# Optimization experiments

Hardware: AMD Instinct MI355X
Metric: run time of the kernel (lower is better)

## Reference

```python
import jax, jax.numpy as jnp
import numpy as np

B, N, C = 4, 20480, 128
H, HD = 8, 16           # num_heads, head_dim (C // H)
L = 4                   # number of WindowBasedGraphAttentionBlocks
NW, WS = 320, 64        # num_windows, window_size (N // NW)
SCALE = HD ** -0.5
EPS = 1e-5


def layernorm(x, g, b):
    mu = jnp.mean(x, axis=-1, keepdims=True)
    var = jnp.mean(jnp.square(x - mu), axis=-1, keepdims=True)
    return (x - mu) * jax.lax.rsqrt(var + EPS) * g + b


def setup_inputs() -> dict:
    key = jax.random.key(0)
    ks = jax.random.split(key, 8)
    x = jax.random.normal(ks[0], (B, N, C), dtype=jnp.float32)
    # geodesic window mapping: each of NW windows has exactly WS members, permuted
    window_ids = jnp.asarray(
        np.random.RandomState(0).permutation(np.repeat(np.arange(NW), WS)),
        dtype=jnp.int32)
    s = 0.02
    inp = {
        'x': x,
        'g1': jnp.ones((L, C), jnp.float32),
        'be1': jnp.zeros((L, C), jnp.float32),
        'Wqkv': jax.random.normal(ks[1], (L, C, 3 * C), jnp.float32) * s,
        'bqkv': jnp.zeros((L, 3 * C), jnp.float32),
        'rel_bias': jax.random.normal(ks[2], (L, H, 1, 1), jnp.float32) * s,
        'Wproj': jax.random.normal(ks[3], (L, C, C), jnp.float32) * s,
        'bproj': jnp.zeros((L, C), jnp.float32),
        'g2': jnp.ones((L, C), jnp.float32),
        'be2': jnp.zeros((L, C), jnp.float32),
        'W1': jax.random.normal(ks[4], (L, C, 4 * C), jnp.float32) * s,
        'b1': jnp.zeros((L, 4 * C), jnp.float32),
        'W2': jax.random.normal(ks[5], (L, 4 * C, C), jnp.float32) * s,
        'b2': jnp.zeros((L, C), jnp.float32),
        'window_ids': window_ids,
    }
    return inp


def _encoder(x, g1, be1, Wqkv, bqkv, rel_bias, Wproj, bproj, g2, be2,
             W1, b1, W2, b2, sort_idx, inv_idx):
    def step(x, p):
        (g1, be1, Wqkv, bqkv, rb, Wp, bp, g2, be2, W1, b1, W2, b2) = p
        shortcut = x
        # GeodesicWindowPartition: gather by argsort(window_ids), split into windows
        win = x[:, sort_idx, :].reshape(B * NW, WS, C)
        h = layernorm(win, g1, be1)
        qkv = (h @ Wqkv + bqkv).reshape(B * NW, WS, 3, H, HD)
        q = qkv[:, :, 0].transpose(0, 2, 1, 3)  # [BW, H, WS, HD]
        k = qkv[:, :, 1].transpose(0, 2, 1, 3)
        v = qkv[:, :, 2].transpose(0, 2, 1, 3)
        attn = jnp.einsum('whqd,whkd->whqk', q, k) * SCALE
        attn = attn + rb[None]                  # relative geometry bias [H,1,1]
        attn = jax.nn.softmax(attn, axis=-1)
        out = jnp.einsum('whqk,whkd->whqd', attn, v)
        out = out.transpose(0, 2, 1, 3).reshape(B * NW, WS, C)
        out = out @ Wp + bp                     # AttentionOutputProjection
        rec = out.reshape(B, N, C)[:, inv_idx, :]  # partition.reverse
        x = shortcut + rec
        h2 = layernorm(x, g2, be2)
        x = x + (jax.nn.gelu(h2 @ W1 + b1) @ W2 + b2)
        return x, None

    params = (g1, be1, Wqkv, bqkv, rel_bias, Wproj, bproj, g2, be2, W1, b1, W2, b2)
    x, _ = jax.lax.scan(step, x, params)
    return x


def reference(x, g1, be1, Wqkv, bqkv, rel_bias, Wproj, bproj, g2, be2,
              W1, b1, W2, b2, window_ids):
    sort_idx = jnp.argsort(window_ids)
    inv_idx = jnp.argsort(sort_idx)
    return _encoder(x, g1, be1, Wqkv, bqkv, rel_bias, Wproj, bproj, g2, be2,
                    W1, b1, W2, b2, sort_idx, inv_idx)
```

## Files before the change

kernel.cpp:

```cpp
#include <hip/hip_runtime.h>
#include <hip/hip_bf16.h>
#include <math.h>

#define Nn 20480
#define Cc 128
#define Hh 8
#define Ll 4
#define NWw 320
#define BN 81920

typedef short sv8 __attribute__((ext_vector_type(8)));
typedef __bf16 bfv8 __attribute__((ext_vector_type(8)));
typedef float f32x4 __attribute__((ext_vector_type(4)));

__device__ __forceinline__ f32x4 mfma16(sv8 a, sv8 b, f32x4 c) {
    return __builtin_amdgcn_mfma_f32_16x16x32_bf16(
        __builtin_bit_cast(bfv8, a), __builtin_bit_cast(bfv8, b), c, 0, 0, 0);
}
__device__ __forceinline__ ushort f2bf(float f) {
    uint u = __float_as_uint(f);
    u += 0x7fffu + ((u >> 16) & 1u);
    return (ushort)(u >> 16);
}
__device__ __forceinline__ float fast_gelu(float x) {
    float z = 0.7978845608f * (x + 0.044715f * x * x * x);
    return x * __builtin_amdgcn_rcpf(1.0f + __expf(-2.0f * z));
}

__global__ __launch_bounds__(64) void rank_kernel(const int* __restrict__ wid,
        int* __restrict__ lrank, int* __restrict__ hist) {
    __shared__ int keys[64];
    int c = blockIdx.x, lane = threadIdx.x;
    for (int j = lane; j < NWw; j += 64) hist[c * NWw + j] = 0;
    int i = c * 64 + lane;
    int w = wid[i];
    keys[lane] = w;
    __syncthreads();
    int rank = 0, total = 0;
    for (int j = 0; j < 64; ++j) {
        int kj = keys[j];
        total += (kj == w);
        rank += (j < lane && kj == w) ? 1 : 0;
    }
    lrank[i] = rank;
    if (rank == 0) hist[c * NWw + w] = total;
}
__global__ __launch_bounds__(64) void prefix_kernel(int* __restrict__ hist) {
    int w = blockIdx.x, lane = threadIdx.x;
    int running = 0;
    for (int it = 0; it < NWw / 64; ++it) {
        int c = it * 64 + lane;
        int v = hist[c * NWw + w];
        int orig = v;
        #pragma unroll
        for (int d = 1; d < 64; d <<= 1) {
            int tt = __shfl_up(v, d, 64);
            if (lane >= d) v += tt;
        }
        hist[c * NWw + w] = running + v - orig;
        running += __shfl(v, 63, 64);
    }
}
__global__ __launch_bounds__(64) void scatter_kernel(const int* __restrict__ wid,
        const int* __restrict__ lrank, const int* __restrict__ hist,
        int* __restrict__ sidx) {
    int c = blockIdx.x, lane = threadIdx.x;
    int i = c * 64 + lane;
    int w = wid[i];
    sidx[w * 64 + hist[c * NWw + w] + lrank[i]] = i;
}

__global__ __launch_bounds__(256) void wconv_kernel(
    const float* __restrict__ Wqkv, const float* __restrict__ Wproj,
    const float* __restrict__ W1, const float* __restrict__ W2,
    ushort* __restrict__ wt) {
    int id = blockIdx.x * 256 + threadIdx.x;
    int l = id / 196608;
    int r = id % 196608;
    const float* src; int dst;
    if (r < 49152) { int n = r % 384, k = r / 384;
        src = Wqkv + l * 49152 + k * 384 + n; dst = l * 196608 + n * 128 + k; }
    else if (r < 65536) { int rr = r - 49152; int n = rr % 128, k = rr / 128;
        src = Wproj + l * 16384 + k * 128 + n; dst = l * 196608 + 49152 + n * 128 + k; }
    else if (r < 131072) { int rr = r - 65536; int n = rr % 512, k = rr / 512;
        src = W1 + l * 65536 + k * 512 + n; dst = l * 196608 + 65536 + n * 128 + k; }
    else { int rr = r - 131072; int n = rr % 128, k = rr / 128;
        src = W2 + l * 65536 + k * 128 + n; dst = l * 196608 + 131072 + n * 512 + k; }
    wt[dst] = f2bf(*src);
}

__global__ __launch_bounds__(256, 2) void attn_fused_kernel(
    const float* __restrict__ xsrc, float* __restrict__ xdst,
    const ushort* __restrict__ wqkvT, const float* __restrict__ bqkv,
    const float* __restrict__ relb, const ushort* __restrict__ wprojT,
    const float* __restrict__ bproj, const float* __restrict__ g1,
    const float* __restrict__ be1, const int* __restrict__ sidx) {
    __shared__ __align__(16) ushort hl_[64][128];
    __shared__ __align__(16) ushort qk_[64][384];
    __shared__ __align__(16) ushort pt[4][16][88];
    __shared__ int ridx[64];

    int t = threadIdx.x;
    int wave = t >> 6, lane = t & 63;
    int lr = lane & 15, lg = lane >> 4;
    int wb = blockIdx.x;
    int bN = (wb / NWw) * Nn;
    int p0 = (wb % NWw) * 64;

    if (t < 64) ridx[t] = sidx[p0 + t];
    __syncthreads();

    {
        int hl2 = lane & 31, hb = lane >> 5;
        float4 gg = *(const float4*)(g1 + hl2 * 4);
        float4 bb = *(const float4*)(be1 + hl2 * 4);
        #pragma unroll
        for (int it = 0; it < 8; ++it) {
            int row = it * 8 + wave * 2 + hb;
            int gi = bN + ridx[row];
            float4 v = *(const float4*)(xsrc + (size_t)gi * Cc + hl2 * 4);
            float s = v.x + v.y + v.z + v.w;
            s += __shfl_xor(s, 1, 64);  s += __shfl_xor(s, 2, 64);
            s += __shfl_xor(s, 4, 64);  s += __shfl_xor(s, 8, 64);
            s += __shfl_xor(s, 16, 64);
            float mu = s * 0.0078125f;
            float d0 = v.x - mu, d1 = v.y - mu, d2 = v.z - mu, d3 = v.w - mu;
            float q = d0 * d0 + d1 * d1 + d2 * d2 + d3 * d3;
            q += __shfl_xor(q, 1, 64);  q += __shfl_xor(q, 2, 64);
            q += __shfl_xor(q, 4, 64);  q += __shfl_xor(q, 8, 64);
            q += __shfl_xor(q, 16, 64);
            float rs = rsqrtf(q * 0.0078125f + 1e-5f);
            uint2 pk;
            pk.x = (uint)f2bf(d0 * rs * gg.x + bb.x) | ((uint)f2bf(d1 * rs * gg.y + bb.y) << 16);
            pk.y = (uint)f2bf(d2 * rs * gg.z + bb.z) | ((uint)f2bf(d3 * rs * gg.w + bb.w) << 16);
            *(uint2*)&hl_[row][(hl2 * 4) ^ ((row & 7) << 3)] = pk;
        }
    }
    __syncthreads();

    {
        f32x4 acc[4][6] = {};
        #pragma unroll
        for (int ks = 0; ks < 4; ++ks) {
            int k0 = ks * 32 + lg * 8;
            sv8 a[4], b[6];
            #pragma unroll
            for (int rf = 0; rf < 4; ++rf) {
                int row = rf * 16 + lr;
                a[rf] = *(const sv8*)&hl_[row][k0 ^ ((row & 7) << 3)];
            }
            #pragma unroll
            for (int nf = 0; nf < 6; ++nf)
                b[nf] = *(const sv8*)(wqkvT + (size_t)(wave * 96 + nf * 16 + lr) * 128 + k0);
            #pragma unroll
            for (int rf = 0; rf < 4; ++rf)
                #pragma unroll
                for (int nf = 0; nf < 6; ++nf)
                    acc[rf][nf] = mfma16(a[rf], b[nf], acc[rf][nf]);
        }
        #pragma unroll
        for (int nf = 0; nf < 6; ++nf) {
            int col = wave * 96 + nf * 16 + lr;
            float bs = bqkv[col];
            #pragma unroll
            for (int rf = 0; rf < 4; ++rf)
                #pragma unroll
                for (int r = 0; r < 4; ++r) {
                    int row = rf * 16 + lg * 4 + r;
                    qk_[row][col ^ ((row & 7) << 3)] = f2bf(acc[rf][nf][r] + bs);
                }
        }
    }
    __syncthreads();

    f32x4 zz = {0.f, 0.f, 0.f, 0.f};
    #pragma unroll
    for (int hi = 0; hi < 2; ++hi) {
        int hh = wave * 2 + hi;
        float rb = relb[hh];
        sv8 bv[2];
        #pragma unroll
        for (int ks = 0; ks < 2; ++ks)
            #pragma unroll
            for (int j = 0; j < 8; ++j) {
                int k = ks * 32 + lg * 8 + j;
                int e = 256 + hh * 16 + lr;
                bv[ks][j] = (short)qk_[k][e ^ ((k & 7) << 3)];
            }
        sv8 aq[4], bk[4];
        sv8 z = {0, 0, 0, 0, 0, 0, 0, 0};
        bool lo = (lg < 2);
        #pragma unroll
        for (int f = 0; f < 4; ++f) {
            aq[f] = z; bk[f] = z;
            if (lo) {
                int row = f * 16 + lr;
                int eq = hh * 16 + lg * 8;
                aq[f] = *(const sv8*)&qk_[row][eq ^ ((row & 7) << 3)];
                int ek = 128 + hh * 16 + lg * 8;
                bk[f] = *(const sv8*)&qk_[row][ek ^ ((row & 7) << 3)];
            }
        }
        f32x4 s[4][4];
        #pragma unroll
        for (int rf = 0; rf < 4; ++rf)
            #pragma unroll
            for (int nf = 0; nf < 4; ++nf)
                s[rf][nf] = mfma16(aq[rf], bk[nf], zz);

        f32x4 o[4];
        #pragma unroll
        for (int rf = 0; rf < 4; ++rf) {
            #pragma unroll
            for (int r = 0; r < 4; ++r) {
                float vv[4];
                float mx = -1e30f;
                #pragma unroll
                for (int nf = 0; nf < 4; ++nf) {
                    float v = s[rf][nf][r] * 0.25f + rb;
                    vv[nf] = v;
                    mx = fmaxf(mx, v);
                }
                mx = fmaxf(mx, __shfl_xor(mx, 1, 64));
                mx = fmaxf(mx, __shfl_xor(mx, 2, 64));
                mx = fmaxf(mx, __shfl_xor(mx, 4, 64));
                mx = fmaxf(mx, __shfl_xor(mx, 8, 64));
                float sum = 0.f;
                #pragma unroll
                for (int nf = 0; nf < 4; ++nf) {
                    float e = __expf(vv[nf] - mx);
                    vv[nf] = e;
                    sum += e;
                }
                sum += __shfl_xor(sum, 1, 64);
                sum += __shfl_xor(sum, 2, 64);
                sum += __shfl_xor(sum, 4, 64);
                sum += __shfl_xor(sum, 8, 64);
                float inv = __builtin_amdgcn_rcpf(sum);
                #pragma unroll
                for (int nf = 0; nf < 4; ++nf)
                    pt[wave][lg * 4 + r][nf * 16 + lr] = f2bf(vv[nf] * inv);
            }
            sv8 ap0 = *(const sv8*)&pt[wave][lr][lg * 8];
            sv8 ap1 = *(const sv8*)&pt[wave][lr][32 + lg * 8];
            o[rf] = mfma16(ap0, bv[0], zz);
            o[rf] = mfma16(ap1, bv[1], o[rf]);
        }
        #pragma unroll
        for (int rf = 0; rf < 4; ++rf)
            #pragma unroll
            for (int r = 0; r < 4; ++r) {
                int row = rf * 16 + lg * 4 + r;
                int e = hh * 16 + lr;
                hl_[row][e ^ ((row & 7) << 3)] = f2bf(o[rf][r]);
            }
    }
    __syncthreads();

    {
        f32x4 acc[4][2] = {};
        #pragma unroll
        for (int ks = 0; ks < 4; ++ks) {
            int k0 = ks * 32 + lg * 8;
            sv8 a[4], b[2];
            #pragma unroll
            for (int rf = 0; rf < 4; ++rf) {
                int row = rf * 16 + lr;
                a[rf] = *(const sv8*)&hl_[row][k0 ^ ((row & 7) << 3)];
            }
            #pragma unroll
            for (int nf = 0; nf < 2; ++nf)
                b[nf] = *(const sv8*)(wprojT + (size_t)(wave * 32 + nf * 16 + lr) * 128 + k0);
            #pragma unroll
            for (int rf = 0; rf < 4; ++rf)
                #pragma unroll
                for (int nf = 0; nf < 2; ++nf)
                    acc[rf][nf] = mfma16(a[rf], b[nf], acc[rf][nf]);
        }
        #pragma unroll
        for (int nf = 0; nf < 2; ++nf) {
            int col = wave * 32 + nf * 16 + lr;
            float bs = bproj[col];
            #pragma unroll
            for (int rf = 0; rf < 4; ++rf)
                #pragma unroll
                for (int r = 0; r < 4; ++r) {
                    int row = rf * 16 + lg * 4 + r;
                    int gi = bN + ridx[row];
                    size_t ad = (size_t)gi * Cc + col;
                    xdst[ad] = xsrc[ad] + acc[rf][nf][r] + bs;
                }
        }
    }
}

__global__ __launch_bounds__(256, 2) void mlp_fused_kernel(
    const float* __restrict__ xsrc, float* __restrict__ xdst,
    const ushort* __restrict__ w1T, const float* __restrict__ b1,
    const ushort* __restrict__ w2T, const float* __restrict__ b2,
    const float* __restrict__ g2, const float* __restrict__ be2) {
    __shared__ __align__(16) ushort hl_[64][128];
    __shared__ __align__(16) ushort hid[64][512];
    int t = threadIdx.x, wave = t >> 6, lane = t & 63;
    int lr = lane & 15, lg = lane >> 4;
    int r0 = blockIdx.x * 64;

    {
        int hl2 = lane & 31, hb = lane >> 5;
        float4 gg = *(const float4*)(g2 + hl2 * 4);
        float4 bb = *(const float4*)(be2 + hl2 * 4);
        #pragma unroll
        for (int it = 0; it < 8; ++it) {
            int row = it * 8 + wave * 2 + hb;
            float4 v = *(const float4*)(xsrc + (size_t)(r0 + row) * Cc + hl2 * 4);
            float s = v.x + v.y + v.z + v.w;
            s += __shfl_xor(s, 1, 64);  s += __shfl_xor(s, 2, 64);
            s += __shfl_xor(s, 4, 64);  s += __shfl_xor(s, 8, 64);
            s += __shfl_xor(s, 16, 64);
            float mu = s * 0.0078125f;
            float d0 = v.x - mu, d1 = v.y - mu, d2 = v.z - mu, d3 = v.w - mu;
            float q = d0 * d0 + d1 * d1 + d2 * d2 + d3 * d3;
            q += __shfl_xor(q, 1, 64);  q += __shfl_xor(q, 2, 64);
            q += __shfl_xor(q, 4, 64);  q += __shfl_xor(q, 8, 64);
            q += __shfl_xor(q, 16, 64);
            float rs = rsqrtf(q * 0.0078125f + 1e-5f);
            uint2 pk;
            pk.x = (uint)f2bf(d0 * rs * gg.x + bb.x) | ((uint)f2bf(d1 * rs * gg.y + bb.y) << 16);
            pk.y = (uint)f2bf(d2 * rs * gg.z + bb.z) | ((uint)f2bf(d3 * rs * gg.w + bb.w) << 16);
            *(uint2*)&hl_[row][(hl2 * 4) ^ ((row & 7) << 3)] = pk;
        }
    }
    __syncthreads();

    {
        f32x4 acc[4][8] = {};
        #pragma unroll
        for (int ks = 0; ks < 4; ++ks) {
            int k0 = ks * 32 + lg * 8;
            sv8 a[4], b[8];
            #pragma unroll
            for (int rf = 0; rf < 4; ++rf) {
                int row = rf * 16 + lr;
                a[rf] = *(const sv8*)&hl_[row][k0 ^ ((row & 7) << 3)];
            }
            #pragma unroll
            for (int nf = 0; nf < 8; ++nf)
                b[nf] = *(const sv8*)(w1T + (size_t)(wave * 128 + nf * 16 + lr) * 128 + k0);
            #pragma unroll
            for (int rf = 0; rf < 4; ++rf)
                #pragma unroll
                for (int nf = 0; nf < 8; ++nf)
                    acc[rf][nf] = mfma16(a[rf], b[nf], acc[rf][nf]);
        }
        #pragma unroll
        for (int nf = 0; nf < 8; ++nf) {
            int col = wave * 128 + nf * 16 + lr;
            float bs = b1[col];
            #pragma unroll
            for (int rf = 0; rf < 4; ++rf)
                #pragma unroll
                for (int r = 0; r < 4; ++r) {
                    int row = rf * 16 + lg * 4 + r;
                    hid[row][col ^ ((row & 7) << 3)] = f2bf(fast_gelu(acc[rf][nf][r] + bs));
                }
        }
    }
    __syncthreads();

    {
        f32x4 acc[4][2] = {};
        #pragma unroll
        for (int ks = 0; ks < 16; ++ks) {
            int k0 = ks * 32 + lg * 8;
            sv8 a[4], b[2];
            #pragma unroll
            for (int rf = 0; rf < 4; ++rf) {
                int row = rf * 16 + lr;
                a[rf] = *(const sv8*)&hid[row][k0 ^ ((row & 7) << 3)];
            }
            #pragma unroll
            for (int nf = 0; nf < 2; ++nf)
                b[nf] = *(const sv8*)(w2T + (size_t)(wave * 32 + nf * 16 + lr) * 512 + k0);
            #pragma unroll
            for (int rf = 0; rf < 4; ++rf)
                #pragma unroll
                for (int nf = 0; nf < 2; ++nf)
                    acc[rf][nf] = mfma16(a[rf], b[nf], acc[rf][nf]);
        }
        #pragma unroll
        for (int nf = 0; nf < 2; ++nf) {
            int col = wave * 32 + nf * 16 + lr;
            float bs = b2[col];
            #pragma unroll
            for (int rf = 0; rf < 4; ++rf)
                #pragma unroll
                for (int r = 0; r < 4; ++r) {
                    int row = rf * 16 + lg * 4 + r;
                    size_t ad = (size_t)(r0 + row) * Cc + col;
                    xdst[ad] = xsrc[ad] + acc[rf][nf][r] + bs;
                }
        }
    }
}

extern "C" void kernel_launch(void* const* d_in, const int* in_sizes, int n_in,
                              void* d_out, int out_size, void* d_ws, size_t ws_size,
                              hipStream_t stream) {
    const float* x_in   = (const float*)d_in[0];
    const float* g1     = (const float*)d_in[1];
    const float* be1    = (const float*)d_in[2];
    const float* Wqkv   = (const float*)d_in[3];
    const float* bqkv   = (const float*)d_in[4];
    const float* relb   = (const float*)d_in[5];
    const float* Wproj  = (const float*)d_in[6];
    const float* bproj  = (const float*)d_in[7];
    const float* g2     = (const float*)d_in[8];
    const float* be2    = (const float*)d_in[9];
    const float* W1     = (const float*)d_in[10];
    const float* b1     = (const float*)d_in[11];
    const float* W2     = (const float*)d_in[12];
    const float* b2     = (const float*)d_in[13];
    const int*   wid    = (const int*)d_in[14];

    size_t off = 0;
    float* x_ws = (float*)d_ws;                      off += (size_t)BN * Cc * 4;
    ushort* wt  = (ushort*)((char*)d_ws + off);      off += (size_t)786432 * 2;
    int* sidx   = (int*)((char*)d_ws + off);         off += (size_t)Nn * 4;
    int* lrank  = (int*)((char*)d_ws + off);         off += (size_t)Nn * 4;
    int* hist   = (int*)((char*)d_ws + off);         off += (size_t)NWw * NWw * 4;
    if (ws_size < off) return;

    rank_kernel<<<Nn / 64, 64, 0, stream>>>(wid, lrank, hist);
    prefix_kernel<<<NWw, 64, 0, stream>>>(hist);
    scatter_kernel<<<Nn / 64, 64, 0, stream>>>(wid, lrank, hist, sidx);
    wconv_kernel<<<786432 / 256, 256, 0, stream>>>(Wqkv, Wproj, W1, W2, wt);

    for (int l = 0; l < Ll; ++l) {
        const ushort* wqkvT  = wt + (size_t)l * 196608;
        const ushort* wprojT = wqkvT + 49152;
        const ushort* w1T    = wqkvT + 65536;
        const ushort* w2T    = wqkvT + 131072;
        const float* xsrc = (l == 0) ? x_in : x_ws;

        attn_fused_kernel<<<BN / 64, 256, 0, stream>>>(
            xsrc, x_ws, wqkvT, bqkv + l * 384, relb + l * Hh,
            wprojT, bproj + l * Cc, g1 + l * Cc, be1 + l * Cc, sidx);

        float* xdst = (l == Ll - 1) ? (float*)d_out : x_ws;
        mlp_fused_kernel<<<BN / 64, 256, 0, stream>>>(
            x_ws, xdst, w1T, b1 + l * 512, w2T, b2 + l * Cc,
            g2 + l * Cc, be2 + l * Cc);
    }
}
```

Before: 524.1 us.

## Store V transposed, compute S^T for in-register softmax, split MLP hidden in halves

Result: slower. 541.4 us (+3.3%).

```diff
diff --git a/kernel.cpp b/kernel.cpp
--- a/kernel.cpp
+++ b/kernel.cpp
@@ -96,8 +96,9 @@
     const float* __restrict__ bproj, const float* __restrict__ g1,
     const float* __restrict__ be1, const int* __restrict__ sidx) {
     __shared__ __align__(16) ushort hl_[64][128];
-    __shared__ __align__(16) ushort qk_[64][384];
-    __shared__ __align__(16) ushort pt[4][16][88];
+    __shared__ __align__(16) ushort qkn[64][256];
+    __shared__ __align__(16) ushort vT[128][76];
+    __shared__ __align__(16) ushort pt[4][16][76];
     __shared__ int ridx[64];
 
     int t = threadIdx.x;
@@ -150,8 +151,12 @@
                 a[rf] = *(const sv8*)&hl_[row][k0 ^ ((row & 7) << 3)];
             }
             #pragma unroll
-            for (int nf = 0; nf < 6; ++nf)
-                b[nf] = *(const sv8*)(wqkvT + (size_t)(wave * 96 + nf * 16 + lr) * 128 + k0);
+            for (int nf = 0; nf < 6; ++nf) {
+                int gcol = (nf < 2 ? 32 * wave + nf * 16
+                          : nf < 4 ? 128 + 32 * wave + (nf - 2) * 16
+                                   : 256 + 32 * wave + (nf - 4) * 16) + lr;
+                b[nf] = *(const sv8*)(wqkvT + (size_t)gcol * 128 + k0);
+            }
             #pragma unroll
             for (int rf = 0; rf < 4; ++rf)
                 #pragma unroll
@@ -160,15 +165,28 @@
         }
         #pragma unroll
         for (int nf = 0; nf < 6; ++nf) {
-            int col = wave * 96 + nf * 16 + lr;
-            float bs = bqkv[col];
-            #pragma unroll
-            for (int rf = 0; rf < 4; ++rf)
-                #pragma unroll
-                for (int r = 0; r < 4; ++r) {
-                    int row = rf * 16 + lg * 4 + r;
-                    qk_[row][col ^ ((row & 7) << 3)] = f2bf(acc[rf][nf][r] + bs);
+            int gcol = (nf < 2 ? 32 * wave + nf * 16
+                      : nf < 4 ? 128 + 32 * wave + (nf - 2) * 16
+                               : 256 + 32 * wave + (nf - 4) * 16) + lr;
+            float bs = bqkv[gcol];
+            if (nf < 4) {
+                #pragma unroll
+                for (int rf = 0; rf < 4; ++rf)
+                    #pragma unroll
+                    for (int r = 0; r < 4; ++r) {
+                        int row = rf * 16 + lg * 4 + r;
+                        qkn[row][gcol ^ ((row & 7) << 3)] = f2bf(acc[rf][nf][r] + bs);
+                    }
+            } else {
+                int dcol = gcol - 256;
+                #pragma unroll
+                for (int rf = 0; rf < 4; ++rf) {
+                    uint2 pk;
+                    pk.x = (uint)f2bf(acc[rf][nf][0] + bs) | ((uint)f2bf(acc[rf][nf][1] + bs) << 16);
+                    pk.y = (uint)f2bf(acc[rf][nf][2] + bs) | ((uint)f2bf(acc[rf][nf][3] + bs) << 16);
+                    *(uint2*)&vT[dcol][rf * 16 + lg * 4] = pk;
                 }
+            }
         }
     }
     __syncthreads();
@@ -181,12 +199,7 @@
         sv8 bv[2];
         #pragma unroll
         for (int ks = 0; ks < 2; ++ks)
-            #pragma unroll
-            for (int j = 0; j < 8; ++j) {
-                int k = ks * 32 + lg * 8 + j;
-                int e = 256 + hh * 16 + lr;
-                bv[ks][j] = (short)qk_[k][e ^ ((k & 7) << 3)];
-            }
+            bv[ks] = *(const sv8*)&vT[hh * 16 + lr][ks * 32 + lg * 8];
         sv8 aq[4], bk[4];
         sv8 z = {0, 0, 0, 0, 0, 0, 0, 0};
         bool lo = (lg < 2);
@@ -195,64 +208,60 @@
             aq[f] = z; bk[f] = z;
             if (lo) {
                 int row = f * 16 + lr;
-                int eq = hh * 16 + lg * 8;
-                aq[f] = *(const sv8*)&qk_[row][eq ^ ((row & 7) << 3)];
-                int ek = 128 + hh * 16 + lg * 8;
-                bk[f] = *(const sv8*)&qk_[row][ek ^ ((row & 7) << 3)];
+                aq[f] = *(const sv8*)&qkn[row][(hh * 16 + lg * 8) ^ ((row & 7) << 3)];
+                bk[f] = *(const sv8*)&qkn[row][(128 + hh * 16 + lg * 8) ^ ((row & 7) << 3)];
             }
         }
         f32x4 s[4][4];
         #pragma unroll
-        for (int rf = 0; rf < 4; ++rf)
-            #pragma unroll
-            for (int nf = 0; nf < 4; ++nf)
-                s[rf][nf] = mfma16(aq[rf], bk[nf], zz);
+        for (int kt = 0; kt < 4; ++kt)
+            #pragma unroll
+            for (int qt = 0; qt < 4; ++qt)
+                s[kt][qt] = mfma16(bk[kt], aq[qt], zz);
 
         f32x4 o[4];
         #pragma unroll
-        for (int rf = 0; rf < 4; ++rf) {
-            #pragma unroll
-            for (int r = 0; r < 4; ++r) {
-                float vv[4];
-                float mx = -1e30f;
-                #pragma unroll
-                for (int nf = 0; nf < 4; ++nf) {
-                    float v = s[rf][nf][r] * 0.25f + rb;
-                    vv[nf] = v;
-                    mx = fmaxf(mx, v);
-                }
-                mx = fmaxf(mx, __shfl_xor(mx, 1, 64));
-                mx = fmaxf(mx, __shfl_xor(mx, 2, 64));
-                mx = fmaxf(mx, __shfl_xor(mx, 4, 64));
-                mx = fmaxf(mx, __shfl_xor(mx, 8, 64));
-                float sum = 0.f;
-                #pragma unroll
-                for (int nf = 0; nf < 4; ++nf) {
-                    float e = __expf(vv[nf] - mx);
-                    vv[nf] = e;
-                    sum += e;
-                }
-                sum += __shfl_xor(sum, 1, 64);
-                sum += __shfl_xor(sum, 2, 64);
-                sum += __shfl_xor(sum, 4, 64);
-                sum += __shfl_xor(sum, 8, 64);
-                float inv = __builtin_amdgcn_rcpf(sum);
-                #pragma unroll
-                for (int nf = 0; nf < 4; ++nf)
-                    pt[wave][lg * 4 + r][nf * 16 + lr] = f2bf(vv[nf] * inv);
+        for (int qt = 0; qt < 4; ++qt) {
+            float v[16];
+            #pragma unroll
+            for (int kt = 0; kt < 4; ++kt)
+                #pragma unroll
+                for (int r = 0; r < 4; ++r)
+                    v[kt * 4 + r] = s[kt][qt][r] * 0.25f + rb;
+            float m0 = fmaxf(fmaxf(fmaxf(v[0], v[1]), fmaxf(v[2], v[3])),
+                             fmaxf(fmaxf(v[4], v[5]), fmaxf(v[6], v[7])));
+            float m1 = fmaxf(fmaxf(fmaxf(v[8], v[9]), fmaxf(v[10], v[11])),
+                             fmaxf(fmaxf(v[12], v[13]), fmaxf(v[14], v[15])));
+            float mx = fmaxf(m0, m1);
+            mx = fmaxf(mx, __shfl_xor(mx, 16, 64));
+            mx = fmaxf(mx, __shfl_xor(mx, 32, 64));
+            float sum = 0.f;
+            #pragma unroll
+            for (int i = 0; i < 16; ++i) {
+                v[i] = __expf(v[i] - mx);
+                sum += v[i];
+            }
+            sum += __shfl_xor(sum, 16, 64);
+            sum += __shfl_xor(sum, 32, 64);
+            float inv = __builtin_amdgcn_rcpf(sum);
+            #pragma unroll
+            for (int kt = 0; kt < 4; ++kt) {
+                uint2 pk;
+                pk.x = (uint)f2bf(v[kt * 4 + 0] * inv) | ((uint)f2bf(v[kt * 4 + 1] * inv) << 16);
+                pk.y = (uint)f2bf(v[kt * 4 + 2] * inv) | ((uint)f2bf(v[kt * 4 + 3] * inv) << 16);
+                *(uint2*)&pt[wave][lr][kt * 16 + lg * 4] = pk;
             }
             sv8 ap0 = *(const sv8*)&pt[wave][lr][lg * 8];
             sv8 ap1 = *(const sv8*)&pt[wave][lr][32 + lg * 8];
-            o[rf] = mfma16(ap0, bv[0], zz);
-            o[rf] = mfma16(ap1, bv[1], o[rf]);
-        }
-        #pragma unroll
-        for (int rf = 0; rf < 4; ++rf)
+            o[qt] = mfma16(ap0, bv[0], zz);
+            o[qt] = mfma16(ap1, bv[1], o[qt]);
+        }
+        #pragma unroll
+        for (int qt = 0; qt < 4; ++qt)
             #pragma unroll
             for (int r = 0; r < 4; ++r) {
-                int row = rf * 16 + lg * 4 + r;
-                int e = hh * 16 + lr;
-                hl_[row][e ^ ((row & 7) << 3)] = f2bf(o[rf][r]);
+                int row = qt * 16 + lg * 4 + r;
+                hl_[row][(hh * 16 + lr) ^ ((row & 7) << 3)] = f2bf(o[qt][r]);
             }
     }
     __syncthreads();
@@ -294,13 +303,13 @@
     }
 }
 
-__global__ __launch_bounds__(256, 2) void mlp_fused_kernel(
+__global__ __launch_bounds__(256, 3) void mlp_fused_kernel(
     const float* __restrict__ xsrc, float* __restrict__ xdst,
     const ushort* __restrict__ w1T, const float* __restrict__ b1,
     const ushort* __restrict__ w2T, const float* __restrict__ b2,
     const float* __restrict__ g2, const float* __restrict__ be2) {
     __shared__ __align__(16) ushort hl_[64][128];
-    __shared__ __align__(16) ushort hid[64][512];
+    __shared__ __align__(16) ushort hid[64][256];
     int t = threadIdx.x, wave = t >> 6, lane = t & 63;
     int lr = lane & 15, lg = lane >> 4;
     int r0 = blockIdx.x * 64;
@@ -332,45 +341,43 @@
     }
     __syncthreads();
 
-    {
-        f32x4 acc[4][8] = {};
+    f32x4 acc2[4][2] = {};
+    #pragma unroll
+    for (int hf = 0; hf < 2; ++hf) {
+        f32x4 acc[4][4] = {};
         #pragma unroll
         for (int ks = 0; ks < 4; ++ks) {
             int k0 = ks * 32 + lg * 8;
-            sv8 a[4], b[8];
+            sv8 a[4], b[4];
             #pragma unroll
             for (int rf = 0; rf < 4; ++rf) {
                 int row = rf * 16 + lr;
                 a[rf] = *(const sv8*)&hl_[row][k0 ^ ((row & 7) << 3)];
             }
             #pragma unroll
-            for (int nf = 0; nf < 8; ++nf)
-                b[nf] = *(const sv8*)(w1T + (size_t)(wave * 128 + nf * 16 + lr) * 128 + k0);
-            #pragma unroll
-            for (int rf = 0; rf < 4; ++rf)
-                #pragma unroll
-                for (int nf = 0; nf < 8; ++nf)
+            for (int nf = 0; nf < 4; ++nf)
+                b[nf] = *(const sv8*)(w1T + (size_t)(hf * 256 + wave * 64 + nf * 16 + lr) * 128 + k0);
+            #pragma unroll
+            for (int rf = 0; rf < 4; ++rf)
+                #pragma unroll
+                for (int nf = 0; nf < 4; ++nf)
                     acc[rf][nf] = mfma16(a[rf], b[nf], acc[rf][nf]);
         }
         #pragma unroll
-        for (int nf = 0; nf < 8; ++nf) {
-            int col = wave * 128 + nf * 16 + lr;
-            float bs = b1[col];
+        for (int nf = 0; nf < 4; ++nf) {
+            int lcol = wave * 64 + nf * 16 + lr;
+            float bs = b1[hf * 256 + lcol];
             #pragma unroll
             for (int rf = 0; rf < 4; ++rf)
                 #pragma unroll
                 for (int r = 0; r < 4; ++r) {
                     int row = rf * 16 + lg * 4 + r;
-                    hid[row][col ^ ((row & 7) << 3)] = f2bf(fast_gelu(acc[rf][nf][r] + bs));
+                    hid[row][lcol ^ ((row & 7) << 3)] = f2bf(fast_gelu(acc[rf][nf][r] + bs));
                 }
         }
-    }
-    __syncthreads();
-
-    {
-        f32x4 acc[4][2] = {};
-        #pragma unroll
-        for (int ks = 0; ks < 16; ++ks) {
+        __syncthreads();
+        #pragma unroll
+        for (int ks = 0; ks < 8; ++ks) {
             int k0 = ks * 32 + lg * 8;
             sv8 a[4], b[2];
             #pragma unroll
@@ -380,26 +387,28 @@
             }
             #pragma unroll
             for (int nf = 0; nf < 2; ++nf)
-                b[nf] = *(const sv8*)(w2T + (size_t)(wave * 32 + nf * 16 + lr) * 512 + k0);
+                b[nf] = *(const sv8*)(w2T + (size_t)(wave * 32 + nf * 16 + lr) * 512 + hf * 256 + k0);
             #pragma unroll
             for (int rf = 0; rf < 4; ++rf)
                 #pragma unroll
                 for (int nf = 0; nf < 2; ++nf)
-                    acc[rf][nf] = mfma16(a[rf], b[nf], acc[rf][nf]);
-        }
-        #pragma unroll
-        for (int nf = 0; nf < 2; ++nf) {
-            int col = wave * 32 + nf * 16 + lr;
-            float bs = b2[col];
-            #pragma unroll
-            for (int rf = 0; rf < 4; ++rf)
-                #pragma unroll
-                for (int r = 0; r < 4; ++r) {
-                    int row = rf * 16 + lg * 4 + r;
-                    size_t ad = (size_t)(r0 + row) * Cc + col;
-                    xdst[ad] = xsrc[ad] + acc[rf][nf][r] + bs;
-                }
-        }
+                    acc2[rf][nf] = mfma16(a[rf], b[nf], acc2[rf][nf]);
+        }
+        if (hf == 0) __syncthreads();
+    }
+
+    #pragma unroll
+    for (int nf = 0; nf < 2; ++nf) {
+        int col = wave * 32 + nf * 16 + lr;
+        float bs = b2[col];
+        #pragma unroll
+        for (int rf = 0; rf < 4; ++rf)
+            #pragma unroll
+            for (int r = 0; r < 4; ++r) {
+                int row = rf * 16 + lg * 4 + r;
+                size_t ad = (size_t)(r0 + row) * Cc + col;
+                xdst[ad] = xsrc[ad] + acc2[rf][nf][r] + bs;
+            }
     }
 }
 
```
